# Kernel tuning notes

Hardware: AMD Instinct MI355X
Metric: run time of the kernel (lower is better)

The kernel has to match this reference:

```python
import jax, jax.numpy as jnp
import numpy as np

EXTENTS = (1, 1, 1)
DIM = 256
HEADS = 8
DH = 32
INNER = HEADS * DH
SCALE = DH ** -0.5
NEG = -1e9


def _windows(t):
    """t: (B, S, H, W, C) -> (B, S, H, W, K, C) local 3D windows, K = prod(2e+1).
    Pads with zeros, window dims flattened in (s, h, w) order (matches unfold i j k)."""
    e = EXTENTS
    B, S, H, W, C = t.shape
    tp = jnp.pad(t, [(0, 0), (e[0], e[0]), (e[1], e[1]), (e[2], e[2]), (0, 0)])
    slabs = []
    for dz in range(2 * e[0] + 1):
        for dy in range(2 * e[1] + 1):
            for dx in range(2 * e[2] + 1):
                slabs.append(tp[:, dz:dz + S, dy:dy + H, dx:dx + W, :])
    return jnp.stack(slabs, axis=4)


def setup_inputs() -> dict:
    key = jax.random.key(0)
    ks = jax.random.split(key, 8)
    B, S, H, W = 2, 8, 32, 32
    scale_w = DIM ** -0.5
    return {
        "x": jax.random.normal(ks[0], (B, S, H, W, DIM), jnp.float32),
        "q": jax.random.normal(ks[1], (B, S, H, W, DIM), jnp.float32),
        "Wq": jax.random.normal(ks[2], (DIM, INNER), jnp.float32) * scale_w,
        "Wk": jax.random.normal(ks[3], (DIM, INNER), jnp.float32) * scale_w,
        "Wv": jax.random.normal(ks[4], (DIM, INNER), jnp.float32) * scale_w,
        "bv": jax.random.normal(ks[5], (INNER,), jnp.float32) * 0.02,
        "Wo": jax.random.normal(ks[6], (INNER, DIM), jnp.float32) * (INNER ** -0.5),
        "bo": jax.random.normal(ks[7], (DIM,), jnp.float32) * 0.02,
    }


def reference(x, q, Wq, Wk, Wv, bv, Wo, bo):
    B, S, H, W, _ = x.shape
    k = x @ Wk                      # (B,S,H,W,INNER)
    v = x @ Wv + bv
    qp = q @ Wq

    kw = _windows(k)                # (B,S,H,W,K,INNER)
    vw = _windows(v)
    K = kw.shape[4]

    # mask: True where window element falls on padding (out of bounds)
    valid = _windows(jnp.ones((1, S, H, W, 1), jnp.float32))[..., 0] > 0  # (1,S,H,W,K)
    mask = ~valid

    qh = qp.reshape(B, S, H, W, HEADS, DH)
    kh = kw.reshape(B, S, H, W, K, HEADS, DH)
    vh = vw.reshape(B, S, H, W, K, HEADS, DH)

    dots = jnp.einsum('bshwnd,bshwknd->bshwnk', qh, kh) * SCALE  # (B,S,H,W,HEADS,K)
    dots = jnp.where(mask[:, :, :, :, None, :], NEG, dots)
    attn = jax.nn.softmax(dots, axis=-1)
    out = jnp.einsum('bshwnk,bshwknd->bshwnd', attn, vh)
    out = out.reshape(B, S, H, W, INNER)
    return out @ Wo + bo            # (B,S,H,W,DIM)
```

## Files before the change

kernel.cpp:

```cpp
#include <hip/hip_runtime.h>
#include <hip/hip_bf16.h>
#include <math.h>

#define B_N 2
#define S_N 8
#define H_N 32
#define W_N 32
#define DIM_N 256
#define NPOS (B_N * S_N * H_N * W_N)
#define NP (NPOS * DIM_N)
#define SCALE_F 0.1767766952966369f

typedef __attribute__((ext_vector_type(8))) short bf16x8;
typedef __attribute__((ext_vector_type(4))) float f32x4;

__device__ __forceinline__ unsigned short f2b(float f) {
    __hip_bfloat16 h = __float2bfloat16(f);
    return __builtin_bit_cast(unsigned short, h);
}
__device__ __forceinline__ unsigned pk2(float a, float b) {
    return (unsigned)f2b(a) | ((unsigned)f2b(b) << 16);
}
__device__ __forceinline__ float bl(unsigned u) { return __uint_as_float(u << 16); }
__device__ __forceinline__ float bh(unsigned u) { return __uint_as_float(u & 0xffff0000u); }

__global__ __launch_bounds__(256)
void wtrans_kernel(const float* __restrict__ Wq, const float* __restrict__ Wk,
                   const float* __restrict__ Wv, const float* __restrict__ Wo,
                   unsigned short* __restrict__ wt)
{
    int mat = blockIdx.y;
    const float* W = (mat == 0) ? Wq : (mat == 1) ? Wk : (mat == 2) ? Wv : Wo;
    unsigned short* Wt = wt + (size_t)mat * 65536;
    int tile = blockIdx.x;
    int tk = tile >> 3, tn = tile & 7;
    __shared__ float t[32][33];
    int c = threadIdx.x & 31;
    int r0 = (threadIdx.x >> 5) * 4;
#pragma unroll
    for (int i = 0; i < 4; ++i)
        t[r0 + i][c] = W[(size_t)(tk * 32 + r0 + i) * 256 + tn * 32 + c];
    __syncthreads();
#pragma unroll
    for (int i = 0; i < 4; ++i)
        Wt[(size_t)(tn * 32 + r0 + i) * 256 + tk * 32 + c] = f2b(t[c][r0 + i]);
}

__global__ __launch_bounds__(512, 4)
void proj_mfma(const float* __restrict__ x, const float* __restrict__ q,
               const unsigned short* __restrict__ wt, const float* __restrict__ bv,
               unsigned short* __restrict__ qh, unsigned short* __restrict__ kh,
               unsigned short* __restrict__ vh)
{
    __shared__ unsigned short Al[64][72];
    __shared__ unsigned short Bl[256][72];

    const int bx = blockIdx.x;
    const int z = bx >> 8;
    const int row0 = (bx & 255) * 64;
    const float* A = (z == 0) ? q : x;
    const unsigned short* Wtm = wt + (size_t)z * 65536;
    unsigned short* outp = (z == 0) ? qh : (z == 1) ? kh : vh;
    const float* bias = (z == 2) ? bv : nullptr;

    const int tid = threadIdx.x;
    const int lane = tid & 63;
    const int wid = tid >> 6;
    const int wm = wid >> 2, wn = wid & 3;
    const int l15 = lane & 15, l4 = lane >> 4;

    f32x4 acc[2][4];
#pragma unroll
    for (int m = 0; m < 2; ++m)
#pragma unroll
        for (int n = 0; n < 4; ++n) acc[m][n] = (f32x4){0.f, 0.f, 0.f, 0.f};

    const int ar = tid >> 3, as = tid & 7;

    for (int kt = 0; kt < DIM_N; kt += 64) {
        {
            const float* p = &A[(size_t)(row0 + ar) * DIM_N + kt + as * 8];
            float4 f0 = *(const float4*)p;
            float4 f1 = *(const float4*)(p + 4);
            uint4 va;
            va.x = pk2(f0.x, f0.y); va.y = pk2(f0.z, f0.w);
            va.z = pk2(f1.x, f1.y); va.w = pk2(f1.z, f1.w);
            *(uint4*)&Al[ar][as * 8] = va;
        }
#pragma unroll
        for (int i = 0; i < 4; ++i) {
            int u = tid + i * 512;
            int rowb = u >> 3, su = u & 7;
            *(uint4*)&Bl[rowb][su * 8] =
                *(const uint4*)&Wtm[(size_t)rowb * DIM_N + kt + su * 8];
        }
        __syncthreads();
#pragma unroll
        for (int ks = 0; ks < 2; ++ks) {
            bf16x8 af[2], bfr[4];
#pragma unroll
            for (int m = 0; m < 2; ++m)
                af[m] = *(const bf16x8*)&Al[wm * 32 + m * 16 + l15][ks * 32 + l4 * 8];
#pragma unroll
            for (int n = 0; n < 4; ++n)
                bfr[n] = *(const bf16x8*)&Bl[wn * 64 + n * 16 + l15][ks * 32 + l4 * 8];
#pragma unroll
            for (int m = 0; m < 2; ++m)
#pragma unroll
                for (int n = 0; n < 4; ++n)
                    acc[m][n] = __builtin_amdgcn_mfma_f32_16x16x32_bf16(
                        af[m], bfr[n], acc[m][n], 0, 0, 0);
        }
        __syncthreads();
    }

#pragma unroll
    for (int n = 0; n < 4; ++n) {
        int col = wn * 64 + n * 16 + l15;
        float bb = bias ? bias[col] : 0.f;
        int head = col >> 5, dh = col & 31;
#pragma unroll
        for (int m = 0; m < 2; ++m) {
#pragma unroll
            for (int rg = 0; rg < 4; ++rg) {
                int row = row0 + wm * 32 + m * 16 + l4 * 4 + rg;
                outp[((size_t)head * NPOS + row) * 32 + dh] =
                    f2b(acc[m][n][rg] + bb);
            }
        }
    }
}

__global__ __launch_bounds__(256, 3)
void attn_fused(const unsigned short* __restrict__ qh, const unsigned short* __restrict__ kh,
                const unsigned short* __restrict__ vh, const unsigned short* __restrict__ wt3,
                const float* __restrict__ bo, float* __restrict__ out)
{
    __shared__ unsigned short aol[32 * 256];
    __shared__ unsigned short Bl[256][72];

    int bix = blockIdx.x;
    int h = bix & 31, s = (bix >> 5) & 7, b = bix >> 8;
    int n = threadIdx.x >> 5;
    int w = threadIdx.x & 31;

    size_t rowbase = (((size_t)b * S_N + s) * H_N + h) * W_N;
    size_t pos = rowbase + w;
    const unsigned short* qrow = qh + ((size_t)n * NPOS + pos) * 32;
    float qv[32];
#pragma unroll
    for (int j = 0; j < 4; ++j) {
        uint4 u = ((const uint4*)qrow)[j];
        qv[j * 8 + 0] = bl(u.x); qv[j * 8 + 1] = bh(u.x);
        qv[j * 8 + 2] = bl(u.y); qv[j * 8 + 3] = bh(u.y);
        qv[j * 8 + 4] = bl(u.z); qv[j * 8 + 5] = bh(u.z);
        qv[j * 8 + 6] = bl(u.w); qv[j * 8 + 7] = bh(u.w);
    }

    float dots[27];
#pragma unroll
    for (int dz = 0; dz < 3; ++dz)
#pragma unroll
        for (int dy = 0; dy < 3; ++dy)
#pragma unroll
            for (int dx = 0; dx < 3; ++dx) {
                int idx = (dz * 3 + dy) * 3 + dx;
                int ns = s + dz - 1, nh = h + dy - 1, nw = w + dx - 1;
                bool ok = (unsigned)ns < S_N && (unsigned)nh < H_N &&
                          (unsigned)nw < W_N;
                float d = -1e30f;
                if (ok) {
                    size_t np = (((size_t)b * S_N + ns) * H_N + nh) * W_N + nw;
                    const unsigned short* krow = kh + ((size_t)n * NPOS + np) * 32;
                    float acc = 0.f;
#pragma unroll
                    for (int j = 0; j < 4; ++j) {
                        uint4 u = ((const uint4*)krow)[j];
                        acc = fmaf(qv[j * 8 + 0], bl(u.x), acc);
                        acc = fmaf(qv[j * 8 + 1], bh(u.x), acc);
                        acc = fmaf(qv[j * 8 + 2], bl(u.y), acc);
                        acc = fmaf(qv[j * 8 + 3], bh(u.y), acc);
                        acc = fmaf(qv[j * 8 + 4], bl(u.z), acc);
                        acc = fmaf(qv[j * 8 + 5], bh(u.z), acc);
                        acc = fmaf(qv[j * 8 + 6], bl(u.w), acc);
                        acc = fmaf(qv[j * 8 + 7], bh(u.w), acc);
                    }
                    d = acc * SCALE_F;
                }
                dots[idx] = d;
            }

    float m = dots[0];
#pragma unroll
    for (int i = 1; i < 27; ++i) m = fmaxf(m, dots[i]);
    float den = 0.f;
#pragma unroll
    for (int i = 0; i < 27; ++i) {
        float p = __expf(dots[i] - m);
        dots[i] = p;
        den += p;
    }
    float inv = 1.f / den;

    float ov[32];
#pragma unroll
    for (int i = 0; i < 32; ++i) ov[i] = 0.f;
#pragma unroll
    for (int dz = 0; dz < 3; ++dz)
#pragma unroll
        for (int dy = 0; dy < 3; ++dy)
#pragma unroll
            for (int dx = 0; dx < 3; ++dx) {
                int idx = (dz * 3 + dy) * 3 + dx;
                int ns = s + dz - 1, nh = h + dy - 1, nw = w + dx - 1;
                bool ok = (unsigned)ns < S_N && (unsigned)nh < H_N &&
                          (unsigned)nw < W_N;
                if (ok) {
                    size_t np = (((size_t)b * S_N + ns) * H_N + nh) * W_N + nw;
                    const unsigned short* vrow = vh + ((size_t)n * NPOS + np) * 32;
                    float p = dots[idx];
#pragma unroll
                    for (int j = 0; j < 4; ++j) {
                        uint4 u = ((const uint4*)vrow)[j];
                        ov[j * 8 + 0] = fmaf(p, bl(u.x), ov[j * 8 + 0]);
                        ov[j * 8 + 1] = fmaf(p, bh(u.x), ov[j * 8 + 1]);
                        ov[j * 8 + 2] = fmaf(p, bl(u.y), ov[j * 8 + 2]);
                        ov[j * 8 + 3] = fmaf(p, bh(u.y), ov[j * 8 + 3]);
                        ov[j * 8 + 4] = fmaf(p, bl(u.z), ov[j * 8 + 4]);
                        ov[j * 8 + 5] = fmaf(p, bh(u.z), ov[j * 8 + 5]);
                        ov[j * 8 + 6] = fmaf(p, bl(u.w), ov[j * 8 + 6]);
                        ov[j * 8 + 7] = fmaf(p, bh(u.w), ov[j * 8 + 7]);
                    }
                }
            }

#pragma unroll
    for (int j = 0; j < 4; ++j) {
        uint4 o;
        o.x = pk2(ov[j * 8 + 0] * inv, ov[j * 8 + 1] * inv);
        o.y = pk2(ov[j * 8 + 2] * inv, ov[j * 8 + 3] * inv);
        o.z = pk2(ov[j * 8 + 4] * inv, ov[j * 8 + 5] * inv);
        o.w = pk2(ov[j * 8 + 6] * inv, ov[j * 8 + 7] * inv);
        int unit = n * 4 + j;
        int su = unit ^ (w & 7);
        *(uint4*)&aol[w * 256 + su * 8] = o;
    }

    const int lane = threadIdx.x & 63;
    const int wv = threadIdx.x >> 6;
    const int l15 = lane & 15, l4 = lane >> 4;

    f32x4 acc[2][4];
#pragma unroll
    for (int m2 = 0; m2 < 2; ++m2)
#pragma unroll
        for (int n2 = 0; n2 < 4; ++n2) acc[m2][n2] = (f32x4){0.f, 0.f, 0.f, 0.f};

    for (int kt = 0; kt < 4; ++kt) {
        __syncthreads();
#pragma unroll
        for (int i = 0; i < 8; ++i) {
            int u = threadIdx.x + i * 256;
            int rowb = u >> 3, su = u & 7;
            *(uint4*)&Bl[rowb][su * 8] =
                *(const uint4*)&wt3[(size_t)rowb * DIM_N + kt * 64 + su * 8];
        }
        __syncthreads();
#pragma unroll
        for (int ks = 0; ks < 2; ++ks) {
            bf16x8 af[2], bfr[4];
#pragma unroll
            for (int m2 = 0; m2 < 2; ++m2) {
                int r = m2 * 16 + l15;
                int unit = kt * 8 + ks * 4 + l4;
                int su = unit ^ (r & 7);
                af[m2] = *(const bf16x8*)&aol[r * 256 + su * 8];
            }
#pragma unroll
            for (int n2 = 0; n2 < 4; ++n2)
                bfr[n2] = *(const bf16x8*)&Bl[wv * 64 + n2 * 16 + l15][ks * 32 + l4 * 8];
#pragma unroll
            for (int m2 = 0; m2 < 2; ++m2)
#pragma unroll
                for (int n2 = 0; n2 < 4; ++n2)
                    acc[m2][n2] = __builtin_amdgcn_mfma_f32_16x16x32_bf16(
                        af[m2], bfr[n2], acc[m2][n2], 0, 0, 0);
        }
    }

#pragma unroll
    for (int n2 = 0; n2 < 4; ++n2) {
        int col = wv * 64 + n2 * 16 + l15;
        float bb = bo[col];
#pragma unroll
        for (int m2 = 0; m2 < 2; ++m2) {
#pragma unroll
            for (int rg = 0; rg < 4; ++rg) {
                int row = m2 * 16 + l4 * 4 + rg;
                out[(rowbase + row) * DIM_N + col] = acc[m2][n2][rg] + bb;
            }
        }
    }
}

extern "C" void kernel_launch(void* const* d_in, const int* in_sizes, int n_in,
                              void* d_out, int out_size, void* d_ws, size_t ws_size,
                              hipStream_t stream)
{
    const float* xin = (const float*)d_in[0];
    const float* qin = (const float*)d_in[1];
    const float* Wq  = (const float*)d_in[2];
    const float* Wk  = (const float*)d_in[3];
    const float* Wv  = (const float*)d_in[4];
    const float* bv  = (const float*)d_in[5];
    const float* Wo  = (const float*)d_in[6];
    const float* bo  = (const float*)d_in[7];
    float* out = (float*)d_out;

    unsigned short* ws = (unsigned short*)d_ws;
    unsigned short* wt = ws;
    unsigned short* qh = wt + (size_t)4 * 65536;
    unsigned short* kh = qh + (size_t)NP;
    unsigned short* vh = kh + (size_t)NP;

    dim3 gw(64, 4);
    wtrans_kernel<<<gw, 256, 0, stream>>>(Wq, Wk, Wv, Wo, wt);

    proj_mfma<<<768, 512, 0, stream>>>(xin, qin, wt, bv, qh, kh, vh);

    attn_fused<<<B_N * S_N * H_N, 256, 0, stream>>>(qh, kh, vh, wt + 3 * 65536, bo, out);
}
```

Baseline: 64.05 us.

## Fuse K and V projections per block and remap attention block order

```diff
diff --git a/kernel.cpp b/kernel.cpp
--- a/kernel.cpp
+++ b/kernel.cpp
@@ -56,12 +56,9 @@
     __shared__ unsigned short Bl[256][72];
 
     const int bx = blockIdx.x;
-    const int z = bx >> 8;
+    const bool is_kv = bx >= 256;
     const int row0 = (bx & 255) * 64;
-    const float* A = (z == 0) ? q : x;
-    const unsigned short* Wtm = wt + (size_t)z * 65536;
-    unsigned short* outp = (z == 0) ? qh : (z == 1) ? kh : vh;
-    const float* bias = (z == 2) ? bv : nullptr;
+    const float* A = is_kv ? x : q;
 
     const int tid = threadIdx.x;
     const int lane = tid & 63;
@@ -69,13 +66,18 @@
     const int wm = wid >> 2, wn = wid & 3;
     const int l15 = lane & 15, l4 = lane >> 4;
 
-    f32x4 acc[2][4];
+    f32x4 accK[2][4], accV[2][4];
 #pragma unroll
     for (int m = 0; m < 2; ++m)
 #pragma unroll
-        for (int n = 0; n < 4; ++n) acc[m][n] = (f32x4){0.f, 0.f, 0.f, 0.f};
+        for (int n = 0; n < 4; ++n) {
+            accK[m][n] = (f32x4){0.f, 0.f, 0.f, 0.f};
+            accV[m][n] = (f32x4){0.f, 0.f, 0.f, 0.f};
+        }
 
     const int ar = tid >> 3, as = tid & 7;
+    const unsigned short* W0 = wt + (is_kv ? 1 : 0) * 65536;
+    const unsigned short* W1 = wt + 2 * 65536;
 
     for (int kt = 0; kt < DIM_N; kt += 64) {
         {
@@ -92,15 +94,18 @@
             int u = tid + i * 512;
             int rowb = u >> 3, su = u & 7;
             *(uint4*)&Bl[rowb][su * 8] =
-                *(const uint4*)&Wtm[(size_t)rowb * DIM_N + kt + su * 8];
+                *(const uint4*)&W0[(size_t)rowb * DIM_N + kt + su * 8];
         }
         __syncthreads();
+        bf16x8 af[2][2];
+#pragma unroll
+        for (int ks = 0; ks < 2; ++ks)
+#pragma unroll
+            for (int m = 0; m < 2; ++m)
+                af[ks][m] = *(const bf16x8*)&Al[wm * 32 + m * 16 + l15][ks * 32 + l4 * 8];
 #pragma unroll
         for (int ks = 0; ks < 2; ++ks) {
-            bf16x8 af[2], bfr[4];
-#pragma unroll
-            for (int m = 0; m < 2; ++m)
-                af[m] = *(const bf16x8*)&Al[wm * 32 + m * 16 + l15][ks * 32 + l4 * 8];
+            bf16x8 bfr[4];
 #pragma unroll
             for (int n = 0; n < 4; ++n)
                 bfr[n] = *(const bf16x8*)&Bl[wn * 64 + n * 16 + l15][ks * 32 + l4 * 8];
@@ -108,8 +113,32 @@
             for (int m = 0; m < 2; ++m)
 #pragma unroll
                 for (int n = 0; n < 4; ++n)
-                    acc[m][n] = __builtin_amdgcn_mfma_f32_16x16x32_bf16(
-                        af[m], bfr[n], acc[m][n], 0, 0, 0);
+                    accK[m][n] = __builtin_amdgcn_mfma_f32_16x16x32_bf16(
+                        af[ks][m], bfr[n], accK[m][n], 0, 0, 0);
+        }
+        if (is_kv) {
+            __syncthreads();
+#pragma unroll
+            for (int i = 0; i < 4; ++i) {
+                int u = tid + i * 512;
+                int rowb = u >> 3, su = u & 7;
+                *(uint4*)&Bl[rowb][su * 8] =
+                    *(const uint4*)&W1[(size_t)rowb * DIM_N + kt + su * 8];
+            }
+            __syncthreads();
+#pragma unroll
+            for (int ks = 0; ks < 2; ++ks) {
+                bf16x8 bfr[4];
+#pragma unroll
+                for (int n = 0; n < 4; ++n)
+                    bfr[n] = *(const bf16x8*)&Bl[wn * 64 + n * 16 + l15][ks * 32 + l4 * 8];
+#pragma unroll
+                for (int m = 0; m < 2; ++m)
+#pragma unroll
+                    for (int n = 0; n < 4; ++n)
+                        accV[m][n] = __builtin_amdgcn_mfma_f32_16x16x32_bf16(
+                            af[ks][m], bfr[n], accV[m][n], 0, 0, 0);
+            }
         }
         __syncthreads();
     }
@@ -117,15 +146,20 @@
 #pragma unroll
     for (int n = 0; n < 4; ++n) {
         int col = wn * 64 + n * 16 + l15;
-        float bb = bias ? bias[col] : 0.f;
         int head = col >> 5, dh = col & 31;
+        float bb = is_kv ? bv[col] : 0.f;
 #pragma unroll
         for (int m = 0; m < 2; ++m) {
 #pragma unroll
             for (int rg = 0; rg < 4; ++rg) {
                 int row = row0 + wm * 32 + m * 16 + l4 * 4 + rg;
-                outp[((size_t)head * NPOS + row) * 32 + dh] =
-                    f2b(acc[m][n][rg] + bb);
+                size_t off = ((size_t)head * NPOS + row) * 32 + dh;
+                if (is_kv) {
+                    kh[off] = f2b(accK[m][n][rg]);
+                    vh[off] = f2b(accV[m][n][rg] + bb);
+                } else {
+                    qh[off] = f2b(accK[m][n][rg]);
+                }
             }
         }
     }
@@ -139,7 +173,8 @@
     __shared__ unsigned short aol[32 * 256];
     __shared__ unsigned short Bl[256][72];
 
-    int bix = blockIdx.x;
+    int p = blockIdx.x;
+    int bix = (p & 7) * 64 + (p >> 3);
     int h = bix & 31, s = (bix >> 5) & 7, b = bix >> 8;
     int n = threadIdx.x >> 5;
     int w = threadIdx.x & 31;
@@ -196,9 +231,9 @@
     float den = 0.f;
 #pragma unroll
     for (int i = 0; i < 27; ++i) {
-        float p = __expf(dots[i] - m);
-        dots[i] = p;
-        den += p;
+        float p2 = __expf(dots[i] - m);
+        dots[i] = p2;
+        den += p2;
     }
     float inv = 1.f / den;
 
@@ -218,18 +253,18 @@
                 if (ok) {
                     size_t np = (((size_t)b * S_N + ns) * H_N + nh) * W_N + nw;
                     const unsigned short* vrow = vh + ((size_t)n * NPOS + np) * 32;
-                    float p = dots[idx];
+                    float pw = dots[idx];
 #pragma unroll
                     for (int j = 0; j < 4; ++j) {
                         uint4 u = ((const uint4*)vrow)[j];
-                        ov[j * 8 + 0] = fmaf(p, bl(u.x), ov[j * 8 + 0]);
-                        ov[j * 8 + 1] = fmaf(p, bh(u.x), ov[j * 8 + 1]);
-                        ov[j * 8 + 2] = fmaf(p, bl(u.y), ov[j * 8 + 2]);
-                        ov[j * 8 + 3] = fmaf(p, bh(u.y), ov[j * 8 + 3]);
-                        ov[j * 8 + 4] = fmaf(p, bl(u.z), ov[j * 8 + 4]);
-                        ov[j * 8 + 5] = fmaf(p, bh(u.z), ov[j * 8 + 5]);
-                        ov[j * 8 + 6] = fmaf(p, bl(u.w), ov[j * 8 + 6]);
-                        ov[j * 8 + 7] = fmaf(p, bh(u.w), ov[j * 8 + 7]);
+                        ov[j * 8 + 0] = fmaf(pw, bl(u.x), ov[j * 8 + 0]);
+                        ov[j * 8 + 1] = fmaf(pw, bh(u.x), ov[j * 8 + 1]);
+                        ov[j * 8 + 2] = fmaf(pw, bl(u.y), ov[j * 8 + 2]);
+                        ov[j * 8 + 3] = fmaf(pw, bh(u.y), ov[j * 8 + 3]);
+                        ov[j * 8 + 4] = fmaf(pw, bl(u.z), ov[j * 8 + 4]);
+                        ov[j * 8 + 5] = fmaf(pw, bh(u.z), ov[j * 8 + 5]);
+                        ov[j * 8 + 6] = fmaf(pw, bl(u.w), ov[j * 8 + 6]);
+                        ov[j * 8 + 7] = fmaf(pw, bh(u.w), ov[j * 8 + 7]);
                     }
                 }
             }
@@ -266,6 +301,7 @@
                 *(const uint4*)&wt3[(size_t)rowb * DIM_N + kt * 64 + su * 8];
         }
         __syncthreads();
+        __builtin_amdgcn_s_setprio(1);
 #pragma unroll
         for (int ks = 0; ks < 2; ++ks) {
             bf16x8 af[2], bfr[4];
@@ -286,6 +322,7 @@
                     acc[m2][n2] = __builtin_amdgcn_mfma_f32_16x16x32_bf16(
                         af[m2], bfr[n2], acc[m2][n2], 0, 0, 0);
         }
+        __builtin_amdgcn_s_setprio(0);
     }
 
 #pragma unroll
@@ -326,7 +363,7 @@
     dim3 gw(64, 4);
     wtrans_kernel<<<gw, 256, 0, stream>>>(Wq, Wk, Wv, Wo, wt);
 
-    proj_mfma<<<768, 512, 0, stream>>>(xin, qin, wt, bv, qh, kh, vh);
+    proj_mfma<<<512, 512, 0, stream>>>(xin, qin, wt, bv, qh, kh, vh);
 
     attn_fused<<<B_N * S_N * H_N, 256, 0, stream>>>(qh, kh, vh, wt + 3 * 65536, bo, out);
 }
```

Result: slower. 72.22 us (+12.8%).

## Batch neighbor K/V row loads, swizzle blocks across XCDs, relax launch bounds

Applied to the files above, without the earlier changes.

```diff
diff --git a/kernel.cpp b/kernel.cpp
--- a/kernel.cpp
+++ b/kernel.cpp
@@ -131,7 +131,7 @@
     }
 }
 
-__global__ __launch_bounds__(256, 3)
+__global__ __launch_bounds__(256, 2)
 void attn_fused(const unsigned short* __restrict__ qh, const unsigned short* __restrict__ kh,
                 const unsigned short* __restrict__ vh, const unsigned short* __restrict__ wt3,
                 const float* __restrict__ bo, float* __restrict__ out)
@@ -139,7 +139,8 @@
     __shared__ unsigned short aol[32 * 256];
     __shared__ unsigned short Bl[256][72];
 
-    int bix = blockIdx.x;
+    int p = blockIdx.x;
+    int bix = (p & 7) * 64 + (p >> 3);
     int h = bix & 31, s = (bix >> 5) & 7, b = bix >> 8;
     int n = threadIdx.x >> 5;
     int w = threadIdx.x & 31;
@@ -161,34 +162,39 @@
 #pragma unroll
     for (int dz = 0; dz < 3; ++dz)
 #pragma unroll
-        for (int dy = 0; dy < 3; ++dy)
+        for (int dy = 0; dy < 3; ++dy) {
+            int ns = s + dz - 1, nh = h + dy - 1;
+            bool rowok = (unsigned)ns < S_N && (unsigned)nh < H_N;
+            size_t rb = rowok ? ((((size_t)b * S_N + ns) * H_N + nh) * W_N)
+                              : rowbase;
+            const unsigned short* base = kh + ((size_t)n * NPOS + rb + w) * 32;
+            uint4 kr[3][4];
 #pragma unroll
             for (int dx = 0; dx < 3; ++dx) {
-                int idx = (dz * 3 + dy) * 3 + dx;
-                int ns = s + dz - 1, nh = h + dy - 1, nw = w + dx - 1;
-                bool ok = (unsigned)ns < S_N && (unsigned)nh < H_N &&
-                          (unsigned)nw < W_N;
-                float d = -1e30f;
-                if (ok) {
-                    size_t np = (((size_t)b * S_N + ns) * H_N + nh) * W_N + nw;
-                    const unsigned short* krow = kh + ((size_t)n * NPOS + np) * 32;
-                    float acc = 0.f;
-#pragma unroll
-                    for (int j = 0; j < 4; ++j) {
-                        uint4 u = ((const uint4*)krow)[j];
-                        acc = fmaf(qv[j * 8 + 0], bl(u.x), acc);
-                        acc = fmaf(qv[j * 8 + 1], bh(u.x), acc);
-                        acc = fmaf(qv[j * 8 + 2], bl(u.y), acc);
-                        acc = fmaf(qv[j * 8 + 3], bh(u.y), acc);
-                        acc = fmaf(qv[j * 8 + 4], bl(u.z), acc);
-                        acc = fmaf(qv[j * 8 + 5], bh(u.z), acc);
-                        acc = fmaf(qv[j * 8 + 6], bl(u.w), acc);
-                        acc = fmaf(qv[j * 8 + 7], bh(u.w), acc);
-                    }
-                    d = acc * SCALE_F;
+                const uint4* kp = (const uint4*)(base + (dx - 1) * 32);
+#pragma unroll
+                for (int j = 0; j < 4; ++j) kr[dx][j] = kp[j];
+            }
+#pragma unroll
+            for (int dx = 0; dx < 3; ++dx) {
+                float acc = 0.f;
+#pragma unroll
+                for (int j = 0; j < 4; ++j) {
+                    uint4 u = kr[dx][j];
+                    acc = fmaf(qv[j * 8 + 0], bl(u.x), acc);
+                    acc = fmaf(qv[j * 8 + 1], bh(u.x), acc);
+                    acc = fmaf(qv[j * 8 + 2], bl(u.y), acc);
+                    acc = fmaf(qv[j * 8 + 3], bh(u.y), acc);
+                    acc = fmaf(qv[j * 8 + 4], bl(u.z), acc);
+                    acc = fmaf(qv[j * 8 + 5], bh(u.z), acc);
+                    acc = fmaf(qv[j * 8 + 6], bl(u.w), acc);
+                    acc = fmaf(qv[j * 8 + 7], bh(u.w), acc);
                 }
-                dots[idx] = d;
-            }
+                int nw = w + dx - 1;
+                bool ok = rowok && (unsigned)nw < W_N;
+                dots[(dz * 3 + dy) * 3 + dx] = ok ? acc * SCALE_F : -1e30f;
+            }
+        }
 
     float m = dots[0];
 #pragma unroll
@@ -196,9 +202,9 @@
     float den = 0.f;
 #pragma unroll
     for (int i = 0; i < 27; ++i) {
-        float p = __expf(dots[i] - m);
-        dots[i] = p;
-        den += p;
+        float p2 = __expf(dots[i] - m);
+        dots[i] = p2;
+        den += p2;
     }
     float inv = 1.f / den;
 
@@ -208,31 +214,36 @@
 #pragma unroll
     for (int dz = 0; dz < 3; ++dz)
 #pragma unroll
-        for (int dy = 0; dy < 3; ++dy)
+        for (int dy = 0; dy < 3; ++dy) {
+            int ns = s + dz - 1, nh = h + dy - 1;
+            bool rowok = (unsigned)ns < S_N && (unsigned)nh < H_N;
+            size_t rb = rowok ? ((((size_t)b * S_N + ns) * H_N + nh) * W_N)
+                              : rowbase;
+            const unsigned short* base = vh + ((size_t)n * NPOS + rb + w) * 32;
+            uint4 vr[3][4];
 #pragma unroll
             for (int dx = 0; dx < 3; ++dx) {
-                int idx = (dz * 3 + dy) * 3 + dx;
-                int ns = s + dz - 1, nh = h + dy - 1, nw = w + dx - 1;
-                bool ok = (unsigned)ns < S_N && (unsigned)nh < H_N &&
-                          (unsigned)nw < W_N;
-                if (ok) {
-                    size_t np = (((size_t)b * S_N + ns) * H_N + nh) * W_N + nw;
-                    const unsigned short* vrow = vh + ((size_t)n * NPOS + np) * 32;
-                    float p = dots[idx];
-#pragma unroll
-                    for (int j = 0; j < 4; ++j) {
-                        uint4 u = ((const uint4*)vrow)[j];
-                        ov[j * 8 + 0] = fmaf(p, bl(u.x), ov[j * 8 + 0]);
-                        ov[j * 8 + 1] = fmaf(p, bh(u.x), ov[j * 8 + 1]);
-                        ov[j * 8 + 2] = fmaf(p, bl(u.y), ov[j * 8 + 2]);
-                        ov[j * 8 + 3] = fmaf(p, bh(u.y), ov[j * 8 + 3]);
-                        ov[j * 8 + 4] = fmaf(p, bl(u.z), ov[j * 8 + 4]);
-                        ov[j * 8 + 5] = fmaf(p, bh(u.z), ov[j * 8 + 5]);
-                        ov[j * 8 + 6] = fmaf(p, bl(u.w), ov[j * 8 + 6]);
-                        ov[j * 8 + 7] = fmaf(p, bh(u.w), ov[j * 8 + 7]);
-                    }
+                const uint4* vp = (const uint4*)(base + (dx - 1) * 32);
+#pragma unroll
+                for (int j = 0; j < 4; ++j) vr[dx][j] = vp[j];
+            }
+#pragma unroll
+            for (int dx = 0; dx < 3; ++dx) {
+                float pw = dots[(dz * 3 + dy) * 3 + dx];
+#pragma unroll
+                for (int j = 0; j < 4; ++j) {
+                    uint4 u = vr[dx][j];
+                    ov[j * 8 + 0] = fmaf(pw, bl(u.x), ov[j * 8 + 0]);
+                    ov[j * 8 + 1] = fmaf(pw, bh(u.x), ov[j * 8 + 1]);
+                    ov[j * 8 + 2] = fmaf(pw, bl(u.y), ov[j * 8 + 2]);
+                    ov[j * 8 + 3] = fmaf(pw, bh(u.y), ov[j * 8 + 3]);
+                    ov[j * 8 + 4] = fmaf(pw, bl(u.z), ov[j * 8 + 4]);
+                    ov[j * 8 + 5] = fmaf(pw, bh(u.z), ov[j * 8 + 5]);
+                    ov[j * 8 + 6] = fmaf(pw, bl(u.w), ov[j * 8 + 6]);
+                    ov[j * 8 + 7] = fmaf(pw, bh(u.w), ov[j * 8 + 7]);
                 }
             }
+        }
 
 #pragma unroll
     for (int j = 0; j < 4; ++j) {
```

Measured after the change: 63.58 us. No clear change (-0.7%).
